# Performance work log

Hardware: AMD Instinct MI355X
Metric: run time of the kernel (lower is better)

Reference implementation:

```python
import jax, jax.numpy as jnp
import numpy as np

B, T, NU, NX = 64, 512, 256, 1024


def setup_inputs() -> dict:
    key = jax.random.key(0)
    ks = jax.random.split(key, 10)
    s = 1.0 / NX  # default uniform_(-1/units, 1/units) init
    w = lambda k, shape: jax.random.uniform(k, shape, jnp.float32, -s, s)
    return {
        "u": jax.random.normal(ks[0], (B, T, NU), jnp.float32),
        "x0": 0.5 * jax.random.normal(ks[1], (B, NX), jnp.float32),
        "Wz": w(ks[2], (NU, NX)), "Uz": w(ks[3], (NX, NX)), "bz": jnp.zeros((NX,), jnp.float32),
        "Wf": w(ks[4], (NU, NX)), "Uf": w(ks[5], (NX, NX)), "bf": jnp.zeros((NX,), jnp.float32),
        "Wr": w(ks[6], (NU, NX)), "Ur": w(ks[7], (NX, NX)), "br": jnp.zeros((NX,), jnp.float32),
    }


def reference(u, x0, Wz, Uz, bz, Wf, Uf, bf, Wr, Ur, br):
    # Precompute input projections for all timesteps (same math, hoisted out of the scan).
    az = jnp.einsum("btu,un->btn", u, Wz) + bz  # (B,T,NX)
    af = jnp.einsum("btu,un->btn", u, Wf) + bf
    ar = jnp.einsum("btu,un->btn", u, Wr) + br
    # time-major for scan
    az, af, ar = (jnp.transpose(a, (1, 0, 2)) for a in (az, af, ar))

    def step(x, inp):
        iz, if_, ir = inp
        z = jax.nn.sigmoid(iz + x @ Uz)            # update gate
        f = jax.nn.sigmoid(if_ + x @ Uf)           # forget gate
        r = jnp.tanh(ir + (f * x) @ Ur)            # squashed candidate
        x_next = z * x + (1.0 - z) * r
        # io_delay=True: output is the state x(k) at the current instant
        return x_next, x

    _, ys = jax.lax.scan(step, x0, (az, af, ar))   # ys: (T,B,NX)
    return jnp.transpose(ys, (1, 0, 2))            # (B,T,NX)
```

## Files before the change

kernel.cpp:

```cpp
#include <hip/hip_runtime.h>
#include <stdint.h>

#define Bsz  64
#define Tsz  512
#define NUsz 256
#define NXsz 1024

#define NGRP 4
#define GWG  64
#define MB   16
#define NC   16

typedef __attribute__((ext_vector_type(8))) short  short8;
typedef __attribute__((ext_vector_type(4))) float  float4v;
typedef unsigned long long ull;

#define FLAGX_OFF   0
#define FLAGFX_OFF  2048
#define XBUF_OFF    4096
#define XBUF_PG     65536
#define FXBUF_OFF   (XBUF_OFF + NGRP * XBUF_PG)

__device__ __forceinline__ short f2bf(float f) {
  unsigned x = __float_as_uint(f);
  return (short)((x + 0x7fffu + ((x >> 16) & 1u)) >> 16);
}

__global__ void gru_init(const float* __restrict__ x0, unsigned char* __restrict__ ws) {
  unsigned idx = blockIdx.x * 256u + threadIdx.x;
  unsigned* flagx  = (unsigned*)(ws + FLAGX_OFF);
  unsigned* flagfx = (unsigned*)(ws + FLAGFX_OFF);
  if (idx < 256u)      flagx[idx] = 1u;
  else if (idx < 512u) flagfx[idx - 256u] = 0u;
  unsigned g = idx >> 14, rem = idx & 16383u;
  unsigned jj = rem >> 8, b = (rem >> 4) & 15u, k = rem & 15u;
  float v = x0[(g * 16u + b) * NXsz + jj * 16u + k];
  *(short*)(ws + XBUF_OFF + g * XBUF_PG + jj * 512u + b * 32u + k * 2u) = f2bf(v);
}

__device__ __forceinline__ void wait_flags(const unsigned* f, int lane, unsigned need) {
  while (true) {
    unsigned v = __hip_atomic_load(f + lane, __ATOMIC_RELAXED, __HIP_MEMORY_SCOPE_AGENT);
    if (__all((int)(v >= need))) break;
    __builtin_amdgcn_s_sleep(1);
  }
  __builtin_amdgcn_fence(__ATOMIC_ACQUIRE, "workgroup");
}

__launch_bounds__(256, 1)
__global__ void gru_persist(const float* __restrict__ u,  const float* __restrict__ x0,
                            const float* __restrict__ Wz, const float* __restrict__ Uz, const float* __restrict__ bz,
                            const float* __restrict__ Wf, const float* __restrict__ Uf, const float* __restrict__ bfp,
                            const float* __restrict__ Wr, const float* __restrict__ Ur, const float* __restrict__ br,
                            float* __restrict__ out, unsigned char* __restrict__ ws)
{
  __shared__ short Ucol[3 * 16 * 1288];
  __shared__ float part[4][2][16][17];
  __shared__ float xs[16][17];
  __shared__ float bz_s[16], bf_s[16], br_s[16];

  const int bx  = blockIdx.x;
  const int xcd = bx & 7;
  const int g   = xcd >> 1;
  const int j   = ((xcd & 1) << 5) | (bx >> 3);
  const int tid = threadIdx.x;
  const int wv  = tid >> 6;
  const int lane = tid & 63;
  const int q   = lane >> 4;
  const int cl  = lane & 15;
  const int col0 = j * NC;

  {
    const float* Us[3] = {Uz, Uf, Ur};
    const float* Wsv[3] = {Wz, Wf, Wr};
    for (int gate = 0; gate < 3; ++gate) {
      short* dst = &Ucol[gate * 20608];
      const float* Ug = Us[gate];
      for (int idx = tid; idx < 16 * 1024; idx += 256) {
        int n = idx & 15, k = idx >> 4;
        dst[n * 1288 + k] = f2bf(Ug[k * NXsz + col0 + n]);
      }
      const float* Wg = Wsv[gate];
      for (int idx = tid; idx < 16 * 256; idx += 256) {
        int n = idx & 15, k = idx >> 4;
        dst[n * 1288 + 1024 + k] = f2bf(Wg[k * NXsz + col0 + n]);
      }
    }
    int b = tid >> 4, n = tid & 15;
    xs[b][n] = x0[(g * MB + b) * NXsz + col0 + n];
    if (tid < 16) {
      bz_s[tid] = bz[col0 + tid];
      bf_s[tid] = bfp[col0 + tid];
      br_s[tid] = br[col0 + tid];
    }
  }
  __syncthreads();

  unsigned* flagx  = (unsigned*)(ws + FLAGX_OFF)  + g * GWG;
  unsigned* flagfx = (unsigned*)(ws + FLAGFX_OFF) + g * GWG;
  unsigned char* xb_base  = ws + XBUF_OFF  + g * XBUF_PG;
  unsigned char* fxb_base = ws + FXBUF_OFF + g * XBUF_PG;

  const short* Uz_l = &Ucol[0 * 20608 + cl * 1288 + q * 8];
  const short* Uf_l = &Ucol[1 * 20608 + cl * 1288 + q * 8];
  const short* Ur_l = &Ucol[2 * 20608 + cl * 1288 + q * 8];
  const unsigned lane_off = (unsigned)(cl * 32 + (q & 1) * 16 + (q >> 1) * 512);

  const int cb  = lane >> 2;
  const int cc0 = (lane & 3) << 2;

  const long uTN = (long)Tsz * NUsz;
  const float* u_row = u + (long)(g * MB + cl) * uTN;

  float zreg[4] = {0.f, 0.f, 0.f, 0.f};

  for (int t = 0; t < Tsz; ++t) {
    const int p = t & 1;
    const unsigned char* xb  = xb_base  + p * 32768;
    unsigned char*       fxb = fxb_base + p * 32768;

    if (wv == 2) {
      #pragma unroll
      for (int r = 0; r < 4; ++r) {
        int row = q * 4 + r;
        out[(long)(g * MB + row) * ((long)Tsz * NXsz) + (long)t * NXsz + col0 + cl] = xs[row][cl];
      }
    }

    short8 au[2];
    #pragma unroll
    for (int i = 0; i < 2; ++i) {
      const float* up = u_row + (long)t * NUsz + (wv * 2 + i) * 32 + q * 8;
      float4v u0 = *(const float4v*)up;
      float4v u1 = *(const float4v*)(up + 4);
      short8 s;
      s[0]=f2bf(u0[0]); s[1]=f2bf(u0[1]); s[2]=f2bf(u0[2]); s[3]=f2bf(u0[3]);
      s[4]=f2bf(u1[0]); s[5]=f2bf(u1[1]); s[6]=f2bf(u1[2]); s[7]=f2bf(u1[3]);
      au[i] = s;
    }
    float4v accz = {0.f,0.f,0.f,0.f}, accf = {0.f,0.f,0.f,0.f};
    #pragma unroll
    for (int i = 0; i < 2; ++i) {
      const int ko = 1024 + (wv * 2 + i) * 32;
      accz = __builtin_amdgcn_mfma_f32_16x16x32_bf16(au[i], *(const short8*)(Uz_l + ko), accz, 0, 0, 0);
      accf = __builtin_amdgcn_mfma_f32_16x16x32_bf16(au[i], *(const short8*)(Uf_l + ko), accf, 0, 0, 0);
    }

    wait_flags(flagx, lane, (unsigned)(t + 1));
    {
      ull ax[16];
      #pragma unroll
      for (int i = 0; i < 8; ++i) {
        const ull* pp = (const ull*)(xb + lane_off + (unsigned)((wv * 8 + i) * 1024));
        ax[2*i]   = __hip_atomic_load(pp,     __ATOMIC_RELAXED, __HIP_MEMORY_SCOPE_AGENT);
        ax[2*i+1] = __hip_atomic_load(pp + 1, __ATOMIC_RELAXED, __HIP_MEMORY_SCOPE_AGENT);
      }
      #pragma unroll
      for (int i = 0; i < 8; ++i) {
        union { ull u2[2]; short8 s8; } cv;
        cv.u2[0] = ax[2*i]; cv.u2[1] = ax[2*i+1];
        const int c = wv * 8 + i;
        accz = __builtin_amdgcn_mfma_f32_16x16x32_bf16(cv.s8, *(const short8*)(Uz_l + 32 * c), accz, 0, 0, 0);
        accf = __builtin_amdgcn_mfma_f32_16x16x32_bf16(cv.s8, *(const short8*)(Uf_l + 32 * c), accf, 0, 0, 0);
      }
    }
    #pragma unroll
    for (int r = 0; r < 4; ++r) {
      part[wv][0][q * 4 + r][cl] = accz[r];
      part[wv][1][q * 4 + r][cl] = accf[r];
    }
    __syncthreads();

    if (wv == 0) {
      #pragma unroll
      for (int jj2 = 0; jj2 < 4; ++jj2) {
        int c = cc0 + jj2;
        float s = part[0][0][cb][c] + part[1][0][cb][c] + part[2][0][cb][c] + part[3][0][cb][c] + bz_s[c];
        zreg[jj2] = 1.f / (1.f + __expf(-s));
      }
    } else if (wv == 1) {
      ull pack = 0;
      #pragma unroll
      for (int jj2 = 0; jj2 < 4; ++jj2) {
        int c = cc0 + jj2;
        float s = part[0][1][cb][c] + part[1][1][cb][c] + part[2][1][cb][c] + part[3][1][cb][c] + bf_s[c];
        float f = 1.f / (1.f + __expf(-s));
        unsigned short h = (unsigned short)f2bf(f * xs[cb][c]);
        pack |= (ull)h << (16 * jj2);
      }
      __hip_atomic_store((ull*)(fxb + j * 512 + cb * 32 + cc0 * 2), pack,
                         __ATOMIC_RELAXED, __HIP_MEMORY_SCOPE_AGENT);
      __builtin_amdgcn_fence(__ATOMIC_RELEASE, "workgroup");
      if (lane == 0)
        __hip_atomic_store(flagfx + j, (unsigned)(t + 1), __ATOMIC_RELAXED, __HIP_MEMORY_SCOPE_AGENT);
    }
    __syncthreads();

    float4v accr = {0.f,0.f,0.f,0.f}, accr2 = {0.f,0.f,0.f,0.f};
    #pragma unroll
    for (int i = 0; i < 2; ++i) {
      const int ko = 1024 + (wv * 2 + i) * 32;
      accr = __builtin_amdgcn_mfma_f32_16x16x32_bf16(au[i], *(const short8*)(Ur_l + ko), accr, 0, 0, 0);
    }
    wait_flags(flagfx, lane, (unsigned)(t + 1));
    {
      ull ax[16];
      #pragma unroll
      for (int i = 0; i < 8; ++i) {
        const ull* pp = (const ull*)(fxb + lane_off + (unsigned)((wv * 8 + i) * 1024));
        ax[2*i]   = __hip_atomic_load(pp,     __ATOMIC_RELAXED, __HIP_MEMORY_SCOPE_AGENT);
        ax[2*i+1] = __hip_atomic_load(pp + 1, __ATOMIC_RELAXED, __HIP_MEMORY_SCOPE_AGENT);
      }
      #pragma unroll
      for (int i = 0; i < 8; ++i) {
        union { ull u2[2]; short8 s8; } cv;
        cv.u2[0] = ax[2*i]; cv.u2[1] = ax[2*i+1];
        short8 b2 = *(const short8*)(Ur_l + 32 * (wv * 8 + i));
        if (i & 1) accr2 = __builtin_amdgcn_mfma_f32_16x16x32_bf16(cv.s8, b2, accr2, 0, 0, 0);
        else       accr  = __builtin_amdgcn_mfma_f32_16x16x32_bf16(cv.s8, b2, accr,  0, 0, 0);
      }
    }
    accr += accr2;
    #pragma unroll
    for (int r = 0; r < 4; ++r)
      part[wv][0][q * 4 + r][cl] = accr[r];
    __syncthreads();

    if (wv == 0) {
      unsigned char* xbn = xb_base + ((t + 1) & 1) * 32768;
      ull pack = 0;
      float xnv[4];
      #pragma unroll
      for (int jj2 = 0; jj2 < 4; ++jj2) {
        int c = cc0 + jj2;
        float s = part[0][0][cb][c] + part[1][0][cb][c] + part[2][0][cb][c] + part[3][0][cb][c] + br_s[c];
        s = fminf(fmaxf(s, -15.f), 15.f);
        float e  = __expf(2.f * s);
        float rr = (e - 1.f) / (e + 1.f);
        float xv = xs[cb][c];
        float xn = zreg[jj2] * xv + (1.f - zreg[jj2]) * rr;
        xnv[jj2] = xn;
        pack |= (ull)(unsigned short)f2bf(xn) << (16 * jj2);
      }
      #pragma unroll
      for (int jj2 = 0; jj2 < 4; ++jj2) xs[cb][cc0 + jj2] = xnv[jj2];
      __hip_atomic_store((ull*)(xbn + j * 512 + cb * 32 + cc0 * 2), pack,
                         __ATOMIC_RELAXED, __HIP_MEMORY_SCOPE_AGENT);
      __builtin_amdgcn_fence(__ATOMIC_RELEASE, "workgroup");
      if (lane == 0)
        __hip_atomic_store(flagx + j, (unsigned)(t + 2), __ATOMIC_RELAXED, __HIP_MEMORY_SCOPE_AGENT);
    }
    __syncthreads();
  }
}

extern "C" void kernel_launch(void* const* d_in, const int* in_sizes, int n_in,
                              void* d_out, int out_size, void* d_ws, size_t ws_size,
                              hipStream_t stream) {
  (void)in_sizes; (void)n_in; (void)out_size; (void)ws_size;
  const float* u   = (const float*)d_in[0];
  const float* x0  = (const float*)d_in[1];
  const float* Wz  = (const float*)d_in[2];
  const float* Uz  = (const float*)d_in[3];
  const float* bz  = (const float*)d_in[4];
  const float* Wf  = (const float*)d_in[5];
  const float* Uf  = (const float*)d_in[6];
  const float* bfp = (const float*)d_in[7];
  const float* Wr  = (const float*)d_in[8];
  const float* Ur  = (const float*)d_in[9];
  const float* br  = (const float*)d_in[10];
  float* out = (float*)d_out;
  unsigned char* ws = (unsigned char*)d_ws;

  hipLaunchKernelGGL(gru_init, dim3(256), dim3(256), 0, stream, x0, ws);

  void* args[] = { (void*)&u, (void*)&x0, (void*)&Wz, (void*)&Uz, (void*)&bz,
                   (void*)&Wf, (void*)&Uf, (void*)&bfp,
                   (void*)&Wr, (void*)&Ur, (void*)&br, (void*)&out, (void*)&ws };
  hipError_t e = hipLaunchCooperativeKernel((const void*)gru_persist, dim3(256), dim3(256),
                                            args, 0, stream);
  if (e != hipSuccess) {
    hipLaunchKernelGGL(gru_persist, dim3(256), dim3(256), 0, stream,
                       u, x0, Wz, Uz, bz, Wf, Uf, bfp, Wr, Ur, br, out, ws);
  }
}
```

Measured before the change: 2.669 ms.

## Replace per-block flag handshakes with tag bits embedded in bf16 data payloads

Drops the separate flag arrays and release fences. Each bf16 value written to the exchange buffers now carries a parity tag in its least-significant mantissa bit, and readers spin on the data itself until every tag matches the expected phase. This removes one store-fence-flag round trip and one flag poll per exchange, and it also removes a __syncthreads by giving the r-gate partials a separate shared buffer. The cost is one bit of bf16 precision, and the scheme relies on each 64-bit store being seen atomically with its tags.

```diff
diff --git a/kernel.cpp b/kernel.cpp
--- a/kernel.cpp
+++ b/kernel.cpp
@@ -15,12 +15,12 @@
 typedef __attribute__((ext_vector_type(4))) float  float4v;
 typedef unsigned long long ull;
 
-#define FLAGX_OFF   0
-#define FLAGFX_OFF  2048
 #define XBUF_OFF    4096
 #define XBUF_PG     65536
 #define FXBUF_OFF   (XBUF_OFF + NGRP * XBUF_PG)
 
+#define TAGM 0x0001000100010001ULL
+
 __device__ __forceinline__ short f2bf(float f) {
   unsigned x = __float_as_uint(f);
   return (short)((x + 0x7fffu + ((x >> 16) & 1u)) >> 16);
@@ -28,23 +28,28 @@
 
 __global__ void gru_init(const float* __restrict__ x0, unsigned char* __restrict__ ws) {
   unsigned idx = blockIdx.x * 256u + threadIdx.x;
-  unsigned* flagx  = (unsigned*)(ws + FLAGX_OFF);
-  unsigned* flagfx = (unsigned*)(ws + FLAGFX_OFF);
-  if (idx < 256u)      flagx[idx] = 1u;
-  else if (idx < 512u) flagfx[idx - 256u] = 0u;
-  unsigned g = idx >> 14, rem = idx & 16383u;
-  unsigned jj = rem >> 8, b = (rem >> 4) & 15u, k = rem & 15u;
-  float v = x0[(g * 16u + b) * NXsz + jj * 16u + k];
-  *(short*)(ws + XBUF_OFF + g * XBUF_PG + jj * 512u + b * 32u + k * 2u) = f2bf(v);
-}
-
-__device__ __forceinline__ void wait_flags(const unsigned* f, int lane, unsigned need) {
-  while (true) {
-    unsigned v = __hip_atomic_load(f + lane, __ATOMIC_RELAXED, __HIP_MEMORY_SCOPE_AGENT);
-    if (__all((int)(v >= need))) break;
-    __builtin_amdgcn_s_sleep(1);
-  }
-  __builtin_amdgcn_fence(__ATOMIC_ACQUIRE, "workgroup");
+  {
+    unsigned g = idx >> 14, rem = idx & 16383u;
+    unsigned jj = rem >> 8, b = (rem >> 4) & 15u, k = rem & 15u;
+    float v = x0[(g * 16u + b) * NXsz + jj * 16u + k];
+    unsigned short h = (unsigned short)f2bf(v) & 0xFFFEu;
+    *(unsigned short*)(ws + XBUF_OFF + g * XBUF_PG + jj * 512u + b * 32u + k * 2u) = h;
+  }
+  if (idx < 16384u) {
+    unsigned g = idx >> 12, o = idx & 4095u;
+    *(ull*)(ws + XBUF_OFF + g * XBUF_PG + 32768u + o * 8u) = TAGM;
+  }
+  if (idx < 32768u) {
+    unsigned g = idx >> 13, o = idx & 8191u;
+    *(ull*)(ws + FXBUF_OFF + g * XBUF_PG + o * 8u) = TAGM;
+  }
+}
+
+__device__ __forceinline__ ull ld_agent(const ull* p) {
+  return __hip_atomic_load(p, __ATOMIC_RELAXED, __HIP_MEMORY_SCOPE_AGENT);
+}
+__device__ __forceinline__ void st_agent(ull* p, ull v) {
+  __hip_atomic_store(p, v, __ATOMIC_RELAXED, __HIP_MEMORY_SCOPE_AGENT);
 }
 
 __launch_bounds__(256, 1)
@@ -56,6 +61,7 @@
 {
   __shared__ short Ucol[3 * 16 * 1288];
   __shared__ float part[4][2][16][17];
+  __shared__ float part2[4][16][17];
   __shared__ float xs[16][17];
   __shared__ float bz_s[16], bf_s[16], br_s[16];
 
@@ -96,8 +102,6 @@
   }
   __syncthreads();
 
-  unsigned* flagx  = (unsigned*)(ws + FLAGX_OFF)  + g * GWG;
-  unsigned* flagfx = (unsigned*)(ws + FLAGFX_OFF) + g * GWG;
   unsigned char* xb_base  = ws + XBUF_OFF  + g * XBUF_PG;
   unsigned char* fxb_base = ws + FXBUF_OFF + g * XBUF_PG;
 
@@ -118,6 +122,9 @@
     const int p = t & 1;
     const unsigned char* xb  = xb_base  + p * 32768;
     unsigned char*       fxb = fxb_base + p * 32768;
+    const unsigned bitx = (unsigned)(t >> 1) & 1u;
+    const unsigned bitn = (unsigned)((t + 1) >> 1) & 1u;
+    const ull wantc = bitx ? TAGM : 0ULL;
 
     if (wv == 2) {
       #pragma unroll
@@ -125,6 +132,14 @@
         int row = q * 4 + r;
         out[(long)(g * MB + row) * ((long)Tsz * NXsz) + (long)t * NXsz + col0 + cl] = xs[row][cl];
       }
+    }
+
+    ull ax[16];
+    #pragma unroll
+    for (int i = 0; i < 8; ++i) {
+      const ull* pp = (const ull*)(xb + lane_off + (unsigned)((wv * 8 + i) * 1024));
+      ax[2*i]   = ld_agent(pp);
+      ax[2*i+1] = ld_agent(pp + 1);
     }
 
     short8 au[2];
@@ -146,23 +161,35 @@
       accf = __builtin_amdgcn_mfma_f32_16x16x32_bf16(au[i], *(const short8*)(Uf_l + ko), accf, 0, 0, 0);
     }
 
-    wait_flags(flagx, lane, (unsigned)(t + 1));
     {
-      ull ax[16];
-      #pragma unroll
-      for (int i = 0; i < 8; ++i) {
-        const ull* pp = (const ull*)(xb + lane_off + (unsigned)((wv * 8 + i) * 1024));
-        ax[2*i]   = __hip_atomic_load(pp,     __ATOMIC_RELAXED, __HIP_MEMORY_SCOPE_AGENT);
-        ax[2*i+1] = __hip_atomic_load(pp + 1, __ATOMIC_RELAXED, __HIP_MEMORY_SCOPE_AGENT);
-      }
-      #pragma unroll
-      for (int i = 0; i < 8; ++i) {
-        union { ull u2[2]; short8 s8; } cv;
-        cv.u2[0] = ax[2*i]; cv.u2[1] = ax[2*i+1];
-        const int c = wv * 8 + i;
-        accz = __builtin_amdgcn_mfma_f32_16x16x32_bf16(cv.s8, *(const short8*)(Uz_l + 32 * c), accz, 0, 0, 0);
-        accf = __builtin_amdgcn_mfma_f32_16x16x32_bf16(cv.s8, *(const short8*)(Uf_l + 32 * c), accf, 0, 0, 0);
-      }
+      unsigned pend = 0xFFu;
+      while (true) {
+        #pragma unroll
+        for (int i = 0; i < 8; ++i) {
+          if (pend & (1u << i)) {
+            if (((ax[2*i] & TAGM) == wantc) && ((ax[2*i+1] & TAGM) == wantc))
+              pend &= ~(1u << i);
+          }
+        }
+        if (__all(pend == 0)) break;
+        __builtin_amdgcn_s_sleep(1);
+        #pragma unroll
+        for (int i = 0; i < 8; ++i) {
+          if (pend & (1u << i)) {
+            const ull* pp = (const ull*)(xb + lane_off + (unsigned)((wv * 8 + i) * 1024));
+            ax[2*i]   = ld_agent(pp);
+            ax[2*i+1] = ld_agent(pp + 1);
+          }
+        }
+      }
+    }
+    #pragma unroll
+    for (int i = 0; i < 8; ++i) {
+      union { ull u2[2]; short8 s8; } cv;
+      cv.u2[0] = ax[2*i]; cv.u2[1] = ax[2*i+1];
+      const int c = wv * 8 + i;
+      accz = __builtin_amdgcn_mfma_f32_16x16x32_bf16(cv.s8, *(const short8*)(Uz_l + 32 * c), accz, 0, 0, 0);
+      accf = __builtin_amdgcn_mfma_f32_16x16x32_bf16(cv.s8, *(const short8*)(Uf_l + 32 * c), accf, 0, 0, 0);
     }
     #pragma unroll
     for (int r = 0; r < 4; ++r) {
@@ -185,45 +212,58 @@
         int c = cc0 + jj2;
         float s = part[0][1][cb][c] + part[1][1][cb][c] + part[2][1][cb][c] + part[3][1][cb][c] + bf_s[c];
         float f = 1.f / (1.f + __expf(-s));
-        unsigned short h = (unsigned short)f2bf(f * xs[cb][c]);
+        unsigned short h = ((unsigned short)f2bf(f * xs[cb][c]) & 0xFFFEu) | (unsigned short)bitx;
         pack |= (ull)h << (16 * jj2);
       }
-      __hip_atomic_store((ull*)(fxb + j * 512 + cb * 32 + cc0 * 2), pack,
-                         __ATOMIC_RELAXED, __HIP_MEMORY_SCOPE_AGENT);
-      __builtin_amdgcn_fence(__ATOMIC_RELEASE, "workgroup");
-      if (lane == 0)
-        __hip_atomic_store(flagfx + j, (unsigned)(t + 1), __ATOMIC_RELAXED, __HIP_MEMORY_SCOPE_AGENT);
-    }
-    __syncthreads();
-
+      st_agent((ull*)(fxb + j * 512 + cb * 32 + cc0 * 2), pack);
+    }
+
+    #pragma unroll
+    for (int i = 0; i < 8; ++i) {
+      const ull* pp = (const ull*)(fxb + lane_off + (unsigned)((wv * 8 + i) * 1024));
+      ax[2*i]   = ld_agent(pp);
+      ax[2*i+1] = ld_agent(pp + 1);
+    }
     float4v accr = {0.f,0.f,0.f,0.f}, accr2 = {0.f,0.f,0.f,0.f};
     #pragma unroll
     for (int i = 0; i < 2; ++i) {
       const int ko = 1024 + (wv * 2 + i) * 32;
       accr = __builtin_amdgcn_mfma_f32_16x16x32_bf16(au[i], *(const short8*)(Ur_l + ko), accr, 0, 0, 0);
     }
-    wait_flags(flagfx, lane, (unsigned)(t + 1));
     {
-      ull ax[16];
-      #pragma unroll
-      for (int i = 0; i < 8; ++i) {
-        const ull* pp = (const ull*)(fxb + lane_off + (unsigned)((wv * 8 + i) * 1024));
-        ax[2*i]   = __hip_atomic_load(pp,     __ATOMIC_RELAXED, __HIP_MEMORY_SCOPE_AGENT);
-        ax[2*i+1] = __hip_atomic_load(pp + 1, __ATOMIC_RELAXED, __HIP_MEMORY_SCOPE_AGENT);
-      }
-      #pragma unroll
-      for (int i = 0; i < 8; ++i) {
-        union { ull u2[2]; short8 s8; } cv;
-        cv.u2[0] = ax[2*i]; cv.u2[1] = ax[2*i+1];
-        short8 b2 = *(const short8*)(Ur_l + 32 * (wv * 8 + i));
-        if (i & 1) accr2 = __builtin_amdgcn_mfma_f32_16x16x32_bf16(cv.s8, b2, accr2, 0, 0, 0);
-        else       accr  = __builtin_amdgcn_mfma_f32_16x16x32_bf16(cv.s8, b2, accr,  0, 0, 0);
-      }
+      unsigned pend = 0xFFu;
+      while (true) {
+        #pragma unroll
+        for (int i = 0; i < 8; ++i) {
+          if (pend & (1u << i)) {
+            if (((ax[2*i] & TAGM) == wantc) && ((ax[2*i+1] & TAGM) == wantc))
+              pend &= ~(1u << i);
+          }
+        }
+        if (__all(pend == 0)) break;
+        __builtin_amdgcn_s_sleep(1);
+        #pragma unroll
+        for (int i = 0; i < 8; ++i) {
+          if (pend & (1u << i)) {
+            const ull* pp = (const ull*)(fxb + lane_off + (unsigned)((wv * 8 + i) * 1024));
+            ax[2*i]   = ld_agent(pp);
+            ax[2*i+1] = ld_agent(pp + 1);
+          }
+        }
+      }
+    }
+    #pragma unroll
+    for (int i = 0; i < 8; ++i) {
+      union { ull u2[2]; short8 s8; } cv;
+      cv.u2[0] = ax[2*i]; cv.u2[1] = ax[2*i+1];
+      short8 b2 = *(const short8*)(Ur_l + 32 * (wv * 8 + i));
+      if (i & 1) accr2 = __builtin_amdgcn_mfma_f32_16x16x32_bf16(cv.s8, b2, accr2, 0, 0, 0);
+      else       accr  = __builtin_amdgcn_mfma_f32_16x16x32_bf16(cv.s8, b2, accr,  0, 0, 0);
     }
     accr += accr2;
     #pragma unroll
     for (int r = 0; r < 4; ++r)
-      part[wv][0][q * 4 + r][cl] = accr[r];
+      part2[wv][q * 4 + r][cl] = accr[r];
     __syncthreads();
 
     if (wv == 0) {
@@ -233,22 +273,18 @@
       #pragma unroll
       for (int jj2 = 0; jj2 < 4; ++jj2) {
         int c = cc0 + jj2;
-        float s = part[0][0][cb][c] + part[1][0][cb][c] + part[2][0][cb][c] + part[3][0][cb][c] + br_s[c];
+        float s = part2[0][cb][c] + part2[1][cb][c] + part2[2][cb][c] + part2[3][cb][c] + br_s[c];
         s = fminf(fmaxf(s, -15.f), 15.f);
         float e  = __expf(2.f * s);
         float rr = (e - 1.f) / (e + 1.f);
         float xv = xs[cb][c];
         float xn = zreg[jj2] * xv + (1.f - zreg[jj2]) * rr;
         xnv[jj2] = xn;
-        pack |= (ull)(unsigned short)f2bf(xn) << (16 * jj2);
+        pack |= (ull)(((unsigned short)f2bf(xn) & 0xFFFEu) | (unsigned short)bitn) << (16 * jj2);
       }
       #pragma unroll
       for (int jj2 = 0; jj2 < 4; ++jj2) xs[cb][cc0 + jj2] = xnv[jj2];
-      __hip_atomic_store((ull*)(xbn + j * 512 + cb * 32 + cc0 * 2), pack,
-                         __ATOMIC_RELAXED, __HIP_MEMORY_SCOPE_AGENT);
-      __builtin_amdgcn_fence(__ATOMIC_RELEASE, "workgroup");
-      if (lane == 0)
-        __hip_atomic_store(flagx + j, (unsigned)(t + 2), __ATOMIC_RELAXED, __HIP_MEMORY_SCOPE_AGENT);
+      st_agent((ull*)(xbn + j * 512 + cb * 32 + cc0 * 2), pack);
     }
     __syncthreads();
   }
```

Result: slower. 3.612 ms (+35.3%).
